# Optimization experiments

Hardware: AMD Instinct MI355X
Metric: run time of the kernel (lower is better)

The kernel has to match this reference:

```python
import jax, jax.numpy as jnp
import numpy as np

TOTAL_MUONS = 2_000_000
BATCH = 16_384
FEAT = 3
COND = 4
NEG = -1.0e9


def _leaky(x):
    return jax.nn.leaky_relu(x, 0.2)


def setup_inputs() -> dict:
    key = jax.random.key(0)
    ks = jax.random.split(key, 12)
    flat_muons = jax.random.normal(ks[0], (TOTAL_MUONS, FEAT), dtype=jnp.float32)
    batch_index = jnp.sort(jax.random.randint(ks[1], (TOTAL_MUONS,), 0, BATCH)).astype(jnp.int64)
    conditions = jax.random.normal(ks[2], (BATCH, COND), dtype=jnp.float32)
    def lin(k, fan_in, fan_out):
        bound = 1.0 / np.sqrt(fan_in)
        kw, kb = jax.random.split(k)
        w = jax.random.uniform(kw, (fan_in, fan_out), jnp.float32, -bound, bound)
        b = jax.random.uniform(kb, (fan_out,), jnp.float32, -bound, bound)
        return w, b
    w1, b1 = lin(ks[3], FEAT + COND, 64)
    w2, b2 = lin(ks[4], 64, 128)
    w3, b3 = lin(ks[5], 128 + COND, 128)
    w4, b4 = lin(ks[6], 128, 1)
    return {"flat_muons": flat_muons, "batch_index": batch_index,
            "conditions": conditions, "batch_size": BATCH,
            "w1": w1, "b1": b1, "w2": w2, "b2": b2,
            "w3": w3, "b3": b3, "w4": w4, "b4": b4}


def reference(flat_muons, batch_index, conditions, batch_size,
              w1, b1, w2, b2, w3, b3, w4, b4):
    # gather event conditions per muon, concat with muon features
    flat_cond = conditions[batch_index]                       # [M, COND]
    point_input = jnp.concatenate([flat_muons, flat_cond], axis=1)
    # point network: Linear -> LeakyReLU(0.2) -> Linear -> LeakyReLU(0.2)
    h = _leaky(point_input @ w1 + b1)
    point_feats = _leaky(h @ w2 + b2)                         # [M, 128]
    point_feats = jnp.nan_to_num(point_feats, nan=0.0, posinf=0.0, neginf=0.0)
    # scatter-reduce amax with init -1e9 (include_self=True semantics)
    seg_max = jax.ops.segment_max(point_feats, batch_index, num_segments=batch_size)
    global_feats = jnp.maximum(seg_max, NEG)                  # [B, 128]
    global_feats = jnp.nan_to_num(global_feats, nan=NEG, posinf=-NEG, neginf=NEG)
    # decision network
    decision_input = jnp.concatenate([global_feats, conditions], axis=1)
    g = _leaky(decision_input @ w3 + b3)
    score = g @ w4 + b4                                       # [B, 1]
    score = score / max(1.0, float(batch_size) ** 0.5)
    return jnp.clip(score, -1000.0, 1000.0)
```

## Files before the change

### kernel.cpp

```cpp
#include <hip/hip_runtime.h>
#include <math.h>

#define NEGF (-1.0e9f)
#define NB 4

typedef __attribute__((ext_vector_type(8))) short short8;
typedef __attribute__((ext_vector_type(4))) float f32x4;

static __device__ __forceinline__ unsigned short bf16_rne(float f) {
    unsigned int u = __float_as_uint(f);
    u += 0x7FFFu + ((u >> 16) & 1u);
    return (unsigned short)(u >> 16);
}

static __device__ __forceinline__ unsigned cvt_pk_bf16(float a, float b) {
    unsigned r;
    asm("v_cvt_pk_bf16_f32 %0, %1, %2" : "=v"(r) : "v"(a), "v"(b));
    return r;
}

__global__ void seg_bounds_kernel(const int* __restrict__ bi, int M, int B,
                                  int* __restrict__ seg) {
    int m = blockIdx.x * blockDim.x + threadIdx.x;
    if (m >= M) return;
    int cur = bi[m];
    if (m == 0) {
        for (int b = 0; b <= cur; ++b) seg[b] = 0;
    } else {
        int prev = bi[m - 1];
        for (int b = prev + 1; b <= cur; ++b) seg[b] = m;
    }
    if (m == M - 1) {
        for (int b = cur + 1; b <= B; ++b) seg[b] = M;
    }
}

__global__ void prep_w2_kernel(const float* __restrict__ w2,
                               unsigned short* __restrict__ wf) {
    int t = blockIdx.x * blockDim.x + threadIdx.x;
    if (t >= 8192) return;
    int e = t & 7, slot = (t >> 3) & 63, ks = (t >> 9) & 1, cg = t >> 10;
    int lane16 = slot & 15, kg = slot >> 4;
    int k = ks * 32 + kg * 8 + e;
    int col = cg * 16 + lane16;
    float w = w2[k * 128 + col];
    unsigned ub = __float_as_uint(w);
    unsigned short hi = (unsigned short)(ub >> 16);
    float lof = w - __uint_as_float(ub & 0xFFFF0000u);
    unsigned short lo = bf16_rne(lof);
    wf[((cg * 2 + ks) * 2 + 0) * 512 + slot * 8 + e] = hi;
    wf[((cg * 2 + ks) * 2 + 1) * 512 + slot * 8 + e] = lo;
}

__global__ __launch_bounds__(128, 3) void critic_kernel(
    const float* __restrict__ muons,
    const float* __restrict__ conds,
    const int*   __restrict__ seg,
    const float* __restrict__ w1,
    const float* __restrict__ b1,
    const unsigned short* __restrict__ w2frag,
    const float* __restrict__ b2,
    const float* __restrict__ w3,
    const float* __restrict__ b3,
    const float* __restrict__ w4,
    const float* __restrict__ b4,
    float* __restrict__ out,
    float scale, int Btot)
{
    __shared__ __align__(16) char  alds[2][4096];
    __shared__ __align__(16) float wpk[64][4];
    __shared__ float din[132];
    __shared__ float red[2];

    const int tid  = threadIdx.x;
    const int wave = tid >> 6;
    const int lane = tid & 63;
    const int l16  = lane & 15;
    const int lkg  = lane >> 4;

    short8 bhi[4][2], blo[4][2];
    {
        const short8* wf = (const short8*)w2frag;
        #pragma unroll
        for (int c = 0; c < 4; ++c) {
            const int cg = wave * 4 + c;
            #pragma unroll
            for (int ks = 0; ks < 2; ++ks) {
                bhi[c][ks] = wf[((cg * 2 + ks) * 2 + 0) * 64 + lane];
                blo[c][ks] = wf[((cg * 2 + ks) * 2 + 1) * 64 + lane];
            }
        }
    }

    const int arow = wave * 16 + (lane >> 2);
    const int ko   = (lane & 3) * 16;
    const unsigned aswz  = (unsigned)((arow & 7) << 4);
    const unsigned wadr0 = ((unsigned)(arow * 128 + ko * 2)) ^ aswz;
    const unsigned wadr1 = ((unsigned)(arow * 128 + ko * 2 + 16)) ^ aswz;

    unsigned rb[2];
    #pragma unroll
    for (int rt = 0; rt < 2; ++rt) {
        const int row = rt * 16 + l16;
        rb[rt] = ((unsigned)(row * 128 + lkg * 16)) ^ ((unsigned)((row & 7) << 4));
    }

    auto l1_write = [&](float x0, float x1, float x2) {
        float hv[16];
        #pragma unroll
        for (int i = 0; i < 16; ++i) {
            const f32x4 wr = *(const f32x4*)&wpk[ko + i][0];
            float s = wr[3];
            s = fmaf(x0, wr[0], s);
            s = fmaf(x1, wr[1], s);
            s = fmaf(x2, wr[2], s);
            hv[i] = fmaxf(s, 0.2f * s);
        }
        unsigned hw[8], lw[8];
        #pragma unroll
        for (int j = 0; j < 8; ++j) {
            const unsigned h = cvt_pk_bf16(hv[2 * j], hv[2 * j + 1]);
            hw[j] = h;
            lw[j] = cvt_pk_bf16(hv[2 * j]     - __uint_as_float(h << 16),
                                hv[2 * j + 1] - __uint_as_float(h & 0xFFFF0000u));
        }
        *(uint4*)(&alds[0][wadr0]) = make_uint4(hw[0], hw[1], hw[2], hw[3]);
        *(uint4*)(&alds[0][wadr1]) = make_uint4(hw[4], hw[5], hw[6], hw[7]);
        *(uint4*)(&alds[1][wadr0]) = make_uint4(lw[0], lw[1], lw[2], lw[3]);
        *(uint4*)(&alds[1][wadr1]) = make_uint4(lw[4], lw[5], lw[6], lw[7]);
    };

    for (int bi = 0; bi < NB; ++bi) {
        const int b = blockIdx.x * NB + bi;
        if (b >= Btot) break;

        const float c0 = conds[b * 4 + 0];
        const float c1 = conds[b * 4 + 1];
        const float c2 = conds[b * 4 + 2];
        const float c3 = conds[b * 4 + 3];
        const int start = seg[b];
        const int end   = seg[b + 1];
        const int nrows = end - start;

        if (tid < 64) {
            float e = b1[tid];
            e = fmaf(c0, w1[3 * 64 + tid], e);
            e = fmaf(c1, w1[4 * 64 + tid], e);
            e = fmaf(c2, w1[5 * 64 + tid], e);
            e = fmaf(c3, w1[6 * 64 + tid], e);
            wpk[tid][0] = w1[0 * 64 + tid];
            wpk[tid][1] = w1[1 * 64 + tid];
            wpk[tid][2] = w1[2 * 64 + tid];
            wpk[tid][3] = e;
        }
        __syncthreads();

        float gmax[4];
        #pragma unroll
        for (int c = 0; c < 4; ++c) gmax[c] = NEGF;

        if (nrows > 0) {
            const int ntiles = (nrows + 31) >> 5;

            if (arow < min(32, nrows)) {
                const int gm = start + arow;
                l1_write(muons[gm * 3 + 0], muons[gm * 3 + 1], muons[gm * 3 + 2]);
            }

            for (int t = 0; t < ntiles; ++t) {
                const int rem = nrows - t * 32;
                const int cnt = min(32, rem);
                __syncthreads();

                float xn0 = 0.f, xn1 = 0.f, xn2 = 0.f;
                bool mv = false;
                if (rem > 32) {
                    mv = arow < min(32, rem - 32);
                    if (mv) {
                        const int gm = start + t * 32 + 32 + arow;
                        xn0 = muons[gm * 3 + 0];
                        xn1 = muons[gm * 3 + 1];
                        xn2 = muons[gm * 3 + 2];
                    }
                }

                #pragma unroll
                for (int rt = 0; rt < 2; ++rt) {
                    const short8 ah0 = *(const short8*)(&alds[0][rb[rt]]);
                    const short8 ah1 = *(const short8*)(&alds[0][rb[rt] ^ 64u]);
                    const short8 al0 = *(const short8*)(&alds[1][rb[rt]]);
                    const short8 al1 = *(const short8*)(&alds[1][rb[rt] ^ 64u]);

                    f32x4 acc[4];
                    __builtin_amdgcn_s_setprio(1);
                    #pragma unroll
                    for (int c = 0; c < 4; ++c) {
                        f32x4 a = (f32x4){0.f, 0.f, 0.f, 0.f};
                        a = __builtin_amdgcn_mfma_f32_16x16x32_bf16(ah0, bhi[c][0], a, 0, 0, 0);
                        a = __builtin_amdgcn_mfma_f32_16x16x32_bf16(ah1, bhi[c][1], a, 0, 0, 0);
                        a = __builtin_amdgcn_mfma_f32_16x16x32_bf16(al0, bhi[c][0], a, 0, 0, 0);
                        a = __builtin_amdgcn_mfma_f32_16x16x32_bf16(al1, bhi[c][1], a, 0, 0, 0);
                        a = __builtin_amdgcn_mfma_f32_16x16x32_bf16(ah0, blo[c][0], a, 0, 0, 0);
                        a = __builtin_amdgcn_mfma_f32_16x16x32_bf16(ah1, blo[c][1], a, 0, 0, 0);
                        acc[c] = a;
                    }
                    __builtin_amdgcn_s_setprio(0);

                    #pragma unroll
                    for (int c = 0; c < 4; ++c)
                        #pragma unroll
                        for (int j = 0; j < 4; ++j) {
                            const int r = rt * 16 + lkg * 4 + j;
                            gmax[c] = fmaxf(gmax[c], (r < cnt) ? acc[c][j] : NEGF);
                        }
                }
                __syncthreads();
                if (mv) l1_write(xn0, xn1, xn2);
            }
        }

        #pragma unroll
        for (int c = 0; c < 4; ++c) {
            float v = gmax[c];
            v = fmaxf(v, __shfl_xor(v, 16, 64));
            v = fmaxf(v, __shfl_xor(v, 32, 64));
            if (lane < 16) {
                const int col = wave * 64 + c * 16 + lane;
                const float biased = v + b2[col];
                const float actv = fmaxf(biased, 0.2f * biased);
                din[col] = (nrows > 0) ? actv : NEGF;
            }
        }
        if (tid < 4) din[128 + tid] = conds[b * 4 + tid];
        __syncthreads();

        float g = b3[tid];
        #pragma unroll 4
        for (int i = 0; i < 132; ++i)
            g = fmaf(din[i], w3[i * 128 + tid], g);
        g = fmaxf(g, 0.2f * g);
        float part = g * w4[tid];
        #pragma unroll
        for (int s = 1; s < 64; s <<= 1)
            part += __shfl_xor(part, s, 64);
        if (lane == 0) red[wave] = part;
        __syncthreads();
        if (tid == 0) {
            float sc = (red[0] + red[1] + b4[0]) * scale;
            out[b] = fminf(fmaxf(sc, -1000.0f), 1000.0f);
        }
    }
}

extern "C" void kernel_launch(void* const* d_in, const int* in_sizes, int n_in,
                              void* d_out, int out_size, void* d_ws, size_t ws_size,
                              hipStream_t stream) {
    const float* muons = (const float*)d_in[0];
    const int*   bidx  = (const int*)d_in[1];
    const float* conds = (const float*)d_in[2];
    const float* w1 = (const float*)d_in[4];
    const float* b1 = (const float*)d_in[5];
    const float* w2 = (const float*)d_in[6];
    const float* b2 = (const float*)d_in[7];
    const float* w3 = (const float*)d_in[8];
    const float* b3 = (const float*)d_in[9];
    const float* w4 = (const float*)d_in[10];
    const float* b4 = (const float*)d_in[11];

    const int M = in_sizes[0] / 3;
    const int B = in_sizes[2] / 4;
    int* seg = (int*)d_ws;
    const size_t off = (((size_t)(B + 1)) * 4 + 255) & ~(size_t)255;
    unsigned short* w2frag = (unsigned short*)((char*)d_ws + off);
    const float scale = 1.0f / fmaxf(1.0f, sqrtf((float)B));

    seg_bounds_kernel<<<(M + 255) / 256, 256, 0, stream>>>(bidx, M, B, seg);
    prep_w2_kernel<<<32, 256, 0, stream>>>(w2, w2frag);
    const int nblk = (B + NB - 1) / NB;
    critic_kernel<<<nblk, 128, 0, stream>>>(muons, conds, seg,
                                            w1, b1, w2frag, b2, w3, b3, w4, b4,
                                            (float*)d_out, scale, B);
}
```

Before: 262.8 us.

## Prefetch muon rows two tiles ahead and use LDS-only barriers

The tile loop now keeps two register buffers of muon coordinates, issuing global loads two tiles ahead of the tile being multiplied. The loop is unrolled by two through a macro to alternate the buffers. Barriers become a custom lgkmcnt(0) wait plus s_barrier, so they no longer wait for the outstanding global prefetches. The wpk table is permuted to reduce LDS bank conflicts in the layer-1 reads, and the decision-layer dot product is split over four accumulators to shorten its dependency chain. A trailing __syncthreads is added to each event iteration; the main risks are higher register pressure and getting the custom barrier ordering wrong.

```diff
diff --git a/kernel.cpp b/kernel.cpp
--- a/kernel.cpp
+++ b/kernel.cpp
@@ -6,6 +6,12 @@
 
 typedef __attribute__((ext_vector_type(8))) short short8;
 typedef __attribute__((ext_vector_type(4))) float f32x4;
+
+#define LGKM_BAR()                                         \
+    do {                                                   \
+        asm volatile("s_waitcnt lgkmcnt(0)" ::: "memory"); \
+        __builtin_amdgcn_s_barrier();                      \
+    } while (0)
 
 static __device__ __forceinline__ unsigned short bf16_rne(float f) {
     unsigned int u = __float_as_uint(f);
@@ -93,10 +99,10 @@
     }
 
     const int arow = wave * 16 + (lane >> 2);
-    const int ko   = (lane & 3) * 16;
+    const int kq   = lane & 3;
     const unsigned aswz  = (unsigned)((arow & 7) << 4);
-    const unsigned wadr0 = ((unsigned)(arow * 128 + ko * 2)) ^ aswz;
-    const unsigned wadr1 = ((unsigned)(arow * 128 + ko * 2 + 16)) ^ aswz;
+    const unsigned wadr0 = ((unsigned)(arow * 128 + kq * 32)) ^ aswz;
+    const unsigned wadr1 = ((unsigned)(arow * 128 + kq * 32 + 16)) ^ aswz;
 
     unsigned rb[2];
     #pragma unroll
@@ -109,7 +115,7 @@
         float hv[16];
         #pragma unroll
         for (int i = 0; i < 16; ++i) {
-            const f32x4 wr = *(const f32x4*)&wpk[ko + i][0];
+            const f32x4 wr = *(const f32x4*)&wpk[i * 4 + kq][0];
             float s = wr[3];
             s = fmaf(x0, wr[0], s);
             s = fmaf(x1, wr[1], s);
@@ -129,6 +135,56 @@
         *(uint4*)(&alds[1][wadr0]) = make_uint4(lw[0], lw[1], lw[2], lw[3]);
         *(uint4*)(&alds[1][wadr1]) = make_uint4(lw[4], lw[5], lw[6], lw[7]);
     };
+
+#define TILE_ITER(TCUR, I0, I1, I2, C0, C1, C2)                             \
+    {                                                                       \
+        const int _t = (TCUR);                                              \
+        LGKM_BAR();                        \
+        I0 = 0.f; I1 = 0.f; I2 = 0.f;                                       \
+        {                                                                   \
+            const int _rem2 = nrows - (_t + 2) * 32;                        \
+            if (_rem2 > 0 && arow < _rem2) {                                \
+                const int _gm = start + (_t + 2) * 32 + arow;               \
+                I0 = muons[_gm * 3 + 0];                                    \
+                I1 = muons[_gm * 3 + 1];                                    \
+                I2 = muons[_gm * 3 + 2];                                    \
+            }                                                               \
+        }                                                                   \
+        const int _cnt = min(32, nrows - _t * 32);                          \
+        _Pragma("unroll")                                                   \
+        for (int rt = 0; rt < 2; ++rt) {                                    \
+            const short8 ah0 = *(const short8*)(&alds[0][rb[rt]]);          \
+            const short8 ah1 = *(const short8*)(&alds[0][rb[rt] ^ 64u]);    \
+            const short8 al0 = *(const short8*)(&alds[1][rb[rt]]);          \
+            const short8 al1 = *(const short8*)(&alds[1][rb[rt] ^ 64u]);    \
+            f32x4 acc[4];                                                   \
+            __builtin_amdgcn_s_setprio(1);                                  \
+            _Pragma("unroll")                                               \
+            for (int c = 0; c < 4; ++c) {                                   \
+                f32x4 a = (f32x4){0.f, 0.f, 0.f, 0.f};                      \
+                a = __builtin_amdgcn_mfma_f32_16x16x32_bf16(ah0, bhi[c][0], a, 0, 0, 0); \
+                a = __builtin_amdgcn_mfma_f32_16x16x32_bf16(ah1, bhi[c][1], a, 0, 0, 0); \
+                a = __builtin_amdgcn_mfma_f32_16x16x32_bf16(al0, bhi[c][0], a, 0, 0, 0); \
+                a = __builtin_amdgcn_mfma_f32_16x16x32_bf16(al1, bhi[c][1], a, 0, 0, 0); \
+                a = __builtin_amdgcn_mfma_f32_16x16x32_bf16(ah0, blo[c][0], a, 0, 0, 0); \
+                a = __builtin_amdgcn_mfma_f32_16x16x32_bf16(ah1, blo[c][1], a, 0, 0, 0); \
+                acc[c] = a;                                                 \
+            }                                                               \
+            __builtin_amdgcn_s_setprio(0);                                  \
+            _Pragma("unroll")                                               \
+            for (int c = 0; c < 4; ++c)                                     \
+                _Pragma("unroll")                                           \
+                for (int j = 0; j < 4; ++j) {                               \
+                    const int r = rt * 16 + lkg * 4 + j;                    \
+                    gmax[c] = fmaxf(gmax[c], (r < _cnt) ? acc[c][j] : NEGF);\
+                }                                                           \
+        }                                                                   \
+        LGKM_BAR();                    \
+        {                                                                   \
+            const int _rem1 = nrows - (_t + 1) * 32;                        \
+            if (_rem1 > 0 && arow < _rem1) l1_write(C0, C1, C2);            \
+        }                                                                   \
+    }
 
     for (int bi = 0; bi < NB; ++bi) {
         const int b = blockIdx.x * NB + bi;
@@ -148,10 +204,11 @@
             e = fmaf(c1, w1[4 * 64 + tid], e);
             e = fmaf(c2, w1[5 * 64 + tid], e);
             e = fmaf(c3, w1[6 * 64 + tid], e);
-            wpk[tid][0] = w1[0 * 64 + tid];
-            wpk[tid][1] = w1[1 * 64 + tid];
-            wpk[tid][2] = w1[2 * 64 + tid];
-            wpk[tid][3] = e;
+            const int p = (tid & 15) * 4 + (tid >> 4);
+            wpk[p][0] = w1[0 * 64 + tid];
+            wpk[p][1] = w1[1 * 64 + tid];
+            wpk[p][2] = w1[2 * 64 + tid];
+            wpk[p][3] = e;
         }
         __syncthreads();
 
@@ -162,61 +219,34 @@
         if (nrows > 0) {
             const int ntiles = (nrows + 31) >> 5;
 
-            if (arow < min(32, nrows)) {
-                const int gm = start + arow;
-                l1_write(muons[gm * 3 + 0], muons[gm * 3 + 1], muons[gm * 3 + 2]);
+            float bA0, bA1, bA2, bB0, bB1, bB2;
+            {
+                float p0 = 0.f, p1 = 0.f, p2 = 0.f;
+                const bool pv = arow < nrows;
+                if (pv) {
+                    const int gm = start + arow;
+                    p0 = muons[gm * 3 + 0];
+                    p1 = muons[gm * 3 + 1];
+                    p2 = muons[gm * 3 + 2];
+                }
+                bB0 = 0.f; bB1 = 0.f; bB2 = 0.f;
+                const int rem1 = nrows - 32;
+                if (rem1 > 0 && arow < rem1) {
+                    const int gm = start + 32 + arow;
+                    bB0 = muons[gm * 3 + 0];
+                    bB1 = muons[gm * 3 + 1];
+                    bB2 = muons[gm * 3 + 2];
+                }
+                if (pv) l1_write(p0, p1, p2);
             }
 
-            for (int t = 0; t < ntiles; ++t) {
-                const int rem = nrows - t * 32;
-                const int cnt = min(32, rem);
-                __syncthreads();
-
-                float xn0 = 0.f, xn1 = 0.f, xn2 = 0.f;
-                bool mv = false;
-                if (rem > 32) {
-                    mv = arow < min(32, rem - 32);
-                    if (mv) {
-                        const int gm = start + t * 32 + 32 + arow;
-                        xn0 = muons[gm * 3 + 0];
-                        xn1 = muons[gm * 3 + 1];
-                        xn2 = muons[gm * 3 + 2];
-                    }
-                }
-
-                #pragma unroll
-                for (int rt = 0; rt < 2; ++rt) {
-                    const short8 ah0 = *(const short8*)(&alds[0][rb[rt]]);
-                    const short8 ah1 = *(const short8*)(&alds[0][rb[rt] ^ 64u]);
-                    const short8 al0 = *(const short8*)(&alds[1][rb[rt]]);
-                    const short8 al1 = *(const short8*)(&alds[1][rb[rt] ^ 64u]);
-
-                    f32x4 acc[4];
-                    __builtin_amdgcn_s_setprio(1);
-                    #pragma unroll
-                    for (int c = 0; c < 4; ++c) {
-                        f32x4 a = (f32x4){0.f, 0.f, 0.f, 0.f};
-                        a = __builtin_amdgcn_mfma_f32_16x16x32_bf16(ah0, bhi[c][0], a, 0, 0, 0);
-                        a = __builtin_amdgcn_mfma_f32_16x16x32_bf16(ah1, bhi[c][1], a, 0, 0, 0);
-                        a = __builtin_amdgcn_mfma_f32_16x16x32_bf16(al0, bhi[c][0], a, 0, 0, 0);
-                        a = __builtin_amdgcn_mfma_f32_16x16x32_bf16(al1, bhi[c][1], a, 0, 0, 0);
-                        a = __builtin_amdgcn_mfma_f32_16x16x32_bf16(ah0, blo[c][0], a, 0, 0, 0);
-                        a = __builtin_amdgcn_mfma_f32_16x16x32_bf16(ah1, blo[c][1], a, 0, 0, 0);
-                        acc[c] = a;
-                    }
-                    __builtin_amdgcn_s_setprio(0);
-
-                    #pragma unroll
-                    for (int c = 0; c < 4; ++c)
-                        #pragma unroll
-                        for (int j = 0; j < 4; ++j) {
-                            const int r = rt * 16 + lkg * 4 + j;
-                            gmax[c] = fmaxf(gmax[c], (r < cnt) ? acc[c][j] : NEGF);
-                        }
-                }
-                __syncthreads();
-                if (mv) l1_write(xn0, xn1, xn2);
+            int t = 0;
+            for (; t + 1 < ntiles; t += 2) {
+                TILE_ITER(t,     bA0, bA1, bA2, bB0, bB1, bB2);
+                TILE_ITER(t + 1, bB0, bB1, bB2, bA0, bA1, bA2);
             }
+            if (t < ntiles)
+                TILE_ITER(t, bA0, bA1, bA2, bB0, bB1, bB2);
         }
 
         #pragma unroll
@@ -232,24 +262,31 @@
             }
         }
         if (tid < 4) din[128 + tid] = conds[b * 4 + tid];
-        __syncthreads();
-
-        float g = b3[tid];
+        LGKM_BAR();
+
+        float g0 = b3[tid], g1 = 0.f, g2 = 0.f, g3 = 0.f;
         #pragma unroll 4
-        for (int i = 0; i < 132; ++i)
-            g = fmaf(din[i], w3[i * 128 + tid], g);
+        for (int i = 0; i < 132; i += 4) {
+            g0 = fmaf(din[i + 0], w3[(i + 0) * 128 + tid], g0);
+            g1 = fmaf(din[i + 1], w3[(i + 1) * 128 + tid], g1);
+            g2 = fmaf(din[i + 2], w3[(i + 2) * 128 + tid], g2);
+            g3 = fmaf(din[i + 3], w3[(i + 3) * 128 + tid], g3);
+        }
+        float g = (g0 + g1) + (g2 + g3);
         g = fmaxf(g, 0.2f * g);
         float part = g * w4[tid];
         #pragma unroll
         for (int s = 1; s < 64; s <<= 1)
             part += __shfl_xor(part, s, 64);
         if (lane == 0) red[wave] = part;
-        __syncthreads();
+        LGKM_BAR();
         if (tid == 0) {
             float sc = (red[0] + red[1] + b4[0]) * scale;
             out[b] = fminf(fmaxf(sc, -1000.0f), 1000.0f);
         }
-    }
+        __syncthreads();
+    }
+#undef TILE_ITER
 }
 
 extern "C" void kernel_launch(void* const* d_in, const int* in_sizes, int n_in,
```

Measured after the change: 285.6 us. 1.09x slower.

## Process 64-row muon tiles per iteration and batch eight events per block

Applied to the files above, without the earlier changes.

The muon tile per loop iteration grows from 32 to 64 rows, so each wave writes two rows into a doubled LDS buffer. The layer-1 weight packing is permuted so each lane handles interleaved output columns, which changes the LDS write addresses. A mask-free max path runs on full tiles, and the decision-layer dot product is split into four independent accumulators to shorten the FMA dependency chain. NB rises to 8, giving fewer, longer blocks. The costs are more LDS per block, more register pressure, and more padded rows wasted on small segments, which matters because segments average about 122 muons.

```diff
diff --git a/kernel.cpp b/kernel.cpp
--- a/kernel.cpp
+++ b/kernel.cpp
@@ -2,7 +2,7 @@
 #include <math.h>
 
 #define NEGF (-1.0e9f)
-#define NB 4
+#define NB 8
 
 typedef __attribute__((ext_vector_type(8))) short short8;
 typedef __attribute__((ext_vector_type(4))) float f32x4;
@@ -67,7 +67,7 @@
     float* __restrict__ out,
     float scale, int Btot)
 {
-    __shared__ __align__(16) char  alds[2][4096];
+    __shared__ __align__(16) char  alds[2][8192];
     __shared__ __align__(16) float wpk[64][4];
     __shared__ float din[132];
     __shared__ float red[2];
@@ -93,23 +93,22 @@
     }
 
     const int arow = wave * 16 + (lane >> 2);
-    const int ko   = (lane & 3) * 16;
+    const int kq   = lane & 3;
     const unsigned aswz  = (unsigned)((arow & 7) << 4);
-    const unsigned wadr0 = ((unsigned)(arow * 128 + ko * 2)) ^ aswz;
-    const unsigned wadr1 = ((unsigned)(arow * 128 + ko * 2 + 16)) ^ aswz;
-
-    unsigned rb[2];
+    const unsigned wadr0 = ((unsigned)(arow * 128 + kq * 32)) ^ aswz;
+
+    unsigned rbA[4];
     #pragma unroll
-    for (int rt = 0; rt < 2; ++rt) {
+    for (int rt = 0; rt < 4; ++rt) {
         const int row = rt * 16 + l16;
-        rb[rt] = ((unsigned)(row * 128 + lkg * 16)) ^ ((unsigned)((row & 7) << 4));
-    }
-
-    auto l1_write = [&](float x0, float x1, float x2) {
+        rbA[rt] = ((unsigned)(row * 128 + lkg * 16)) ^ ((unsigned)((row & 7) << 4));
+    }
+
+    auto l1_write = [&](float x0, float x1, float x2, unsigned wa) {
         float hv[16];
         #pragma unroll
         for (int i = 0; i < 16; ++i) {
-            const f32x4 wr = *(const f32x4*)&wpk[ko + i][0];
+            const f32x4 wr = *(const f32x4*)&wpk[i * 4 + kq][0];
             float s = wr[3];
             s = fmaf(x0, wr[0], s);
             s = fmaf(x1, wr[1], s);
@@ -124,10 +123,10 @@
             lw[j] = cvt_pk_bf16(hv[2 * j]     - __uint_as_float(h << 16),
                                 hv[2 * j + 1] - __uint_as_float(h & 0xFFFF0000u));
         }
-        *(uint4*)(&alds[0][wadr0]) = make_uint4(hw[0], hw[1], hw[2], hw[3]);
-        *(uint4*)(&alds[0][wadr1]) = make_uint4(hw[4], hw[5], hw[6], hw[7]);
-        *(uint4*)(&alds[1][wadr0]) = make_uint4(lw[0], lw[1], lw[2], lw[3]);
-        *(uint4*)(&alds[1][wadr1]) = make_uint4(lw[4], lw[5], lw[6], lw[7]);
+        *(uint4*)(&alds[0][wa])        = make_uint4(hw[0], hw[1], hw[2], hw[3]);
+        *(uint4*)(&alds[0][wa ^ 16u])  = make_uint4(hw[4], hw[5], hw[6], hw[7]);
+        *(uint4*)(&alds[1][wa])        = make_uint4(lw[0], lw[1], lw[2], lw[3]);
+        *(uint4*)(&alds[1][wa ^ 16u])  = make_uint4(lw[4], lw[5], lw[6], lw[7]);
     };
 
     for (int bi = 0; bi < NB; ++bi) {
@@ -148,10 +147,11 @@
             e = fmaf(c1, w1[4 * 64 + tid], e);
             e = fmaf(c2, w1[5 * 64 + tid], e);
             e = fmaf(c3, w1[6 * 64 + tid], e);
-            wpk[tid][0] = w1[0 * 64 + tid];
-            wpk[tid][1] = w1[1 * 64 + tid];
-            wpk[tid][2] = w1[2 * 64 + tid];
-            wpk[tid][3] = e;
+            const int p = (tid & 15) * 4 + (tid >> 4);
+            wpk[p][0] = w1[0 * 64 + tid];
+            wpk[p][1] = w1[1 * 64 + tid];
+            wpk[p][2] = w1[2 * 64 + tid];
+            wpk[p][3] = e;
         }
         __syncthreads();
 
@@ -160,36 +160,50 @@
         for (int c = 0; c < 4; ++c) gmax[c] = NEGF;
 
         if (nrows > 0) {
-            const int ntiles = (nrows + 31) >> 5;
-
-            if (arow < min(32, nrows)) {
-                const int gm = start + arow;
-                l1_write(muons[gm * 3 + 0], muons[gm * 3 + 1], muons[gm * 3 + 2]);
+            const int ntiles = (nrows + 63) >> 6;
+
+            {
+                if (arow < nrows) {
+                    const int gm = start + arow;
+                    l1_write(muons[gm * 3 + 0], muons[gm * 3 + 1],
+                             muons[gm * 3 + 2], wadr0);
+                }
+                if (arow + 32 < nrows) {
+                    const int gm = start + arow + 32;
+                    l1_write(muons[gm * 3 + 0], muons[gm * 3 + 1],
+                             muons[gm * 3 + 2], wadr0 + 4096u);
+                }
             }
 
             for (int t = 0; t < ntiles; ++t) {
-                const int rem = nrows - t * 32;
-                const int cnt = min(32, rem);
+                const int rem = nrows - t * 64;
+                const int cnt = min(64, rem);
                 __syncthreads();
 
-                float xn0 = 0.f, xn1 = 0.f, xn2 = 0.f;
-                bool mv = false;
-                if (rem > 32) {
-                    mv = arow < min(32, rem - 32);
-                    if (mv) {
-                        const int gm = start + t * 32 + 32 + arow;
-                        xn0 = muons[gm * 3 + 0];
-                        xn1 = muons[gm * 3 + 1];
-                        xn2 = muons[gm * 3 + 2];
-                    }
+                const int rem1 = rem - 64;
+                float pA0 = 0.f, pA1 = 0.f, pA2 = 0.f;
+                float pB0 = 0.f, pB1 = 0.f, pB2 = 0.f;
+                const bool vA = arow < rem1;
+                const bool vB = arow + 32 < rem1;
+                if (vA) {
+                    const int gm = start + (t + 1) * 64 + arow;
+                    pA0 = muons[gm * 3 + 0];
+                    pA1 = muons[gm * 3 + 1];
+                    pA2 = muons[gm * 3 + 2];
+                }
+                if (vB) {
+                    const int gm = start + (t + 1) * 64 + arow + 32;
+                    pB0 = muons[gm * 3 + 0];
+                    pB1 = muons[gm * 3 + 1];
+                    pB2 = muons[gm * 3 + 2];
                 }
 
                 #pragma unroll
-                for (int rt = 0; rt < 2; ++rt) {
-                    const short8 ah0 = *(const short8*)(&alds[0][rb[rt]]);
-                    const short8 ah1 = *(const short8*)(&alds[0][rb[rt] ^ 64u]);
-                    const short8 al0 = *(const short8*)(&alds[1][rb[rt]]);
-                    const short8 al1 = *(const short8*)(&alds[1][rb[rt] ^ 64u]);
+                for (int rt = 0; rt < 4; ++rt) {
+                    const short8 ah0 = *(const short8*)(&alds[0][rbA[rt]]);
+                    const short8 ah1 = *(const short8*)(&alds[0][rbA[rt] ^ 64u]);
+                    const short8 al0 = *(const short8*)(&alds[1][rbA[rt]]);
+                    const short8 al1 = *(const short8*)(&alds[1][rbA[rt] ^ 64u]);
 
                     f32x4 acc[4];
                     __builtin_amdgcn_s_setprio(1);
@@ -206,16 +220,26 @@
                     }
                     __builtin_amdgcn_s_setprio(0);
 
-                    #pragma unroll
-                    for (int c = 0; c < 4; ++c)
+                    if (cnt == 64) {
                         #pragma unroll
-                        for (int j = 0; j < 4; ++j) {
-                            const int r = rt * 16 + lkg * 4 + j;
-                            gmax[c] = fmaxf(gmax[c], (r < cnt) ? acc[c][j] : NEGF);
-                        }
+                        for (int c = 0; c < 4; ++c)
+                            #pragma unroll
+                            for (int j = 0; j < 4; ++j)
+                                gmax[c] = fmaxf(gmax[c], acc[c][j]);
+                    } else {
+                        #pragma unroll
+                        for (int c = 0; c < 4; ++c)
+                            #pragma unroll
+                            for (int j = 0; j < 4; ++j) {
+                                const int r = rt * 16 + lkg * 4 + j;
+                                gmax[c] = fmaxf(gmax[c],
+                                                (r < cnt) ? acc[c][j] : NEGF);
+                            }
+                    }
                 }
                 __syncthreads();
-                if (mv) l1_write(xn0, xn1, xn2);
+                if (vA) l1_write(pA0, pA1, pA2, wadr0);
+                if (vB) l1_write(pB0, pB1, pB2, wadr0 + 4096u);
             }
         }
 
@@ -234,10 +258,15 @@
         if (tid < 4) din[128 + tid] = conds[b * 4 + tid];
         __syncthreads();
 
-        float g = b3[tid];
+        float g0 = b3[tid], g1 = 0.f, g2 = 0.f, g3 = 0.f;
         #pragma unroll 4
-        for (int i = 0; i < 132; ++i)
-            g = fmaf(din[i], w3[i * 128 + tid], g);
+        for (int i = 0; i < 132; i += 4) {
+            g0 = fmaf(din[i + 0], w3[(i + 0) * 128 + tid], g0);
+            g1 = fmaf(din[i + 1], w3[(i + 1) * 128 + tid], g1);
+            g2 = fmaf(din[i + 2], w3[(i + 2) * 128 + tid], g2);
+            g3 = fmaf(din[i + 3], w3[(i + 3) * 128 + tid], g3);
+        }
+        float g = (g0 + g1) + (g2 + g3);
         g = fmaxf(g, 0.2f * g);
         float part = g * w4[tid];
         #pragma unroll
```

Measured after the change: 278.6 us. 1.06x slower.
